# Kernel optimization log

Hardware: AMD Instinct MI355X
Metric: run time of the kernel (lower is better)

## Reference

```python
import jax, jax.numpy as jnp
import numpy as np
import math

B, CH, BINS, W = 2, 8, 1024, 1024
FF = 2048
BANDS = 4
HD = BINS // BANDS
EPS = 1e-5


def _ln(x, g, b):
    m = jnp.mean(x, -1, keepdims=True)
    v = jnp.mean(jnp.square(x - m), -1, keepdims=True)
    return (x - m) * jax.lax.rsqrt(v + EPS) * g + b


def _conv1d(x, w, pad, groups=1):
    # x: [B, C, W], w: [O, I/groups, k]
    return jax.lax.conv_general_dilated(x, w, (1,), [(pad, pad)],
                                        dimension_numbers=('NCH', 'OIH', 'NCH'),
                                        feature_group_count=groups)


def _attn(h, mem, qw, qb, qcw, qcb, kw, kb, kcw, kcb, vw, vb, vcw, vcb, ow, ob, er):
    b, w, c = h.shape

    def proj(src, lw, lb, cw, cb):
        y = src @ lw.T + lb                                   # [b, w, c]
        y = _conv1d(y.transpose(0, 2, 1), cw, 1, groups=c) + cb[None, :, None]
        return y.transpose(0, 2, 1)                           # [b, w, c]

    q = proj(h, qw, qb, qcw, qcb).reshape(b, w, BANDS, HD).transpose(0, 2, 1, 3)   # [b, n, w, hd]
    k = proj(mem, kw, kb, kcw, kcb).reshape(b, w, BANDS, HD).transpose(0, 2, 1, 3)
    v = proj(mem, vw, vb, vcw, vcb).reshape(b, w, BANDS, HD).transpose(0, 2, 1, 3)
    # relative position bias via Music-Transformer pad/skew trick
    p = jnp.einsum('bnwh,hc->bnwc', q, er)                    # [b, n, w, W]
    p = jnp.pad(p, ((0, 0), (0, 0), (0, 0), (1, 0))).transpose(0, 1, 3, 2)[:, :, 1:, :]
    qk = (jnp.einsum('bnqh,bnkh->bnqk', q, k) + p) / math.sqrt(c)
    a = jax.nn.softmax(qk, axis=-1)
    o = jnp.einsum('bnqk,bnkh->bnqh', a, v).transpose(0, 2, 1, 3).reshape(b, w, c)
    return o @ ow.T + ob


def _forward(x, w_in, ln1_g, ln1_b, glu_w, ln2_g, ln2_b, c1L_w, c1R_w, ln3_g, ln3_b,
             c1M_dw, c1M_pw, ln4_g, ln4_b, qw, qb, qcw, qcb, kw, kb, kcw, kcb,
             vw, vb, vcw, vcb, ow, ob, er, ln5_g, ln5_b, c2_w, c3_w):
    # in_project: Linear(channels, 1, bias=False) on x.transpose(1,3), squeeze
    xf = jnp.einsum('bcfw,c->bwf', x, w_in)                   # [B, W, BINS]
    # GLU block
    h = _ln(xf, ln1_g, ln1_b)
    g = h @ glu_w.T
    ga, gb = jnp.split(g, 2, axis=-1)
    xf = xf + ga * jax.nn.sigmoid(gb)
    # conv feedforward block
    h = _ln(xf, ln2_g, ln2_b)
    hL = jax.nn.relu(h @ c1L_w.T)                             # [B, W, FF]
    hR = jax.nn.relu(_conv1d(h.transpose(0, 2, 1), c1R_w, 1)).transpose(0, 2, 1)  # [B, W, FF//4]
    hR = jnp.pad(hR, ((0, 0), (0, 0), (0, FF - FF // 4)))
    h = _ln(hL + hR, ln3_g, ln3_b)
    h = _conv1d(_conv1d(h.transpose(0, 2, 1), c1M_dw, 4, groups=FF), c1M_pw, 0).transpose(0, 2, 1)
    xf = xf + h
    # multiband attention
    h = _ln(xf, ln4_g, ln4_b)
    h = _attn(h, h, qw, qb, qcw, qcb, kw, kb, kcw, kcb, vw, vb, vcw, vcb, ow, ob, er)
    xf = xf + h
    # squared-relu FFN
    h = _ln(xf, ln5_g, ln5_b)
    h = jnp.square(jax.nn.relu(h @ c2_w.T)) @ c3_w.T
    xf = xf + h
    return xf.transpose(0, 2, 1)[:, None, :, :]               # [B, 1, BINS, W]


def setup_inputs() -> dict:
    key = jax.random.key(0)
    keys = iter(jax.random.split(key, 48))

    def n(shape, s=0.02):
        return jax.random.normal(next(keys), shape, dtype=jnp.float32) * s

    ones = lambda d: jnp.ones((d,), jnp.float32)
    zeros = lambda d: jnp.zeros((d,), jnp.float32)
    return {
        'x': jax.random.normal(next(keys), (B, CH, BINS, W), dtype=jnp.float32),
        'w_in': n((CH,)),
        'ln1_g': ones(BINS), 'ln1_b': zeros(BINS),
        'glu_w': n((2 * BINS, BINS)),
        'ln2_g': ones(BINS), 'ln2_b': zeros(BINS),
        'c1L_w': n((FF, BINS)),
        'c1R_w': n((FF // 4, BINS, 3)),
        'ln3_g': ones(FF), 'ln3_b': zeros(FF),
        'c1M_dw': n((FF, 1, 9)),
        'c1M_pw': n((BINS, FF, 1)),
        'ln4_g': ones(BINS), 'ln4_b': zeros(BINS),
        'qw': n((BINS, BINS)), 'qb': zeros(BINS), 'qcw': n((BINS, 1, 3)), 'qcb': zeros(BINS),
        'kw': n((BINS, BINS)), 'kb': zeros(BINS), 'kcw': n((BINS, 1, 3)), 'kcb': zeros(BINS),
        'vw': n((BINS, BINS)), 'vb': zeros(BINS), 'vcw': n((BINS, 1, 3)), 'vcb': zeros(BINS),
        'ow': n((BINS, BINS)), 'ob': zeros(BINS),
        'er': n((HD, W), s=1.0),
        'ln5_g': ones(BINS), 'ln5_b': zeros(BINS),
        'c2_w': n((FF, BINS)), 'c3_w': n((BINS, FF)),
    }


def reference(x, w_in, ln1_g, ln1_b, glu_w, ln2_g, ln2_b, c1L_w, c1R_w, ln3_g, ln3_b,
              c1M_dw, c1M_pw, ln4_g, ln4_b, qw, qb, qcw, qcb, kw, kb, kcw, kcb,
              vw, vb, vcw, vcb, ow, ob, er, ln5_g, ln5_b, c2_w, c3_w):
    return _forward(x, w_in, ln1_g, ln1_b, glu_w, ln2_g, ln2_b, c1L_w, c1R_w, ln3_g, ln3_b,
                    c1M_dw, c1M_pw, ln4_g, ln4_b, qw, qb, qcw, qcb, kw, kb, kcw, kcb,
                    vw, vb, vcw, vcb, ow, ob, er, ln5_g, ln5_b, c2_w, c3_w)
```

## Files before the change

### kernel.cpp

```cpp
#include <hip/hip_runtime.h>


typedef float f32x4 __attribute__((ext_vector_type(4)));
typedef short short8 __attribute__((ext_vector_type(8)));
typedef unsigned short u16;
typedef unsigned int u32;

__device__ __forceinline__ float bf2f(u16 u){
  u32 v = ((u32)u) << 16;
  return __builtin_bit_cast(float, v);
}
__device__ __forceinline__ u16 f2bf(float f){
  u32 u = __builtin_bit_cast(u32, f);
  u32 r = (u + 0x7fffu + ((u >> 16) & 1u)) >> 16;
  return (u16)r;
}
__device__ __forceinline__ u32 pack2(float a, float b){
  return (u32)f2bf(a) | ((u32)f2bf(b) << 16);
}
__device__ __forceinline__ void unpack8(uint4 u, float* f){
  f[0]=bf2f(u.x & 0xffffu); f[1]=bf2f(u.x >> 16);
  f[2]=bf2f(u.y & 0xffffu); f[3]=bf2f(u.y >> 16);
  f[4]=bf2f(u.z & 0xffffu); f[5]=bf2f(u.z >> 16);
  f[6]=bf2f(u.w & 0xffffu); f[7]=bf2f(u.w >> 16);
}

__device__ __forceinline__ void gload16(const u16* g, u16* l){
  __builtin_amdgcn_global_load_lds(
      (const __attribute__((address_space(1))) unsigned int*)g,
      (__attribute__((address_space(3))) unsigned int*)l, 16, 0, 0);
}
template<int N> __device__ __forceinline__ void waitvm(){
  asm volatile("s_waitcnt vmcnt(%0)" :: "n"(N) : "memory");
}
__device__ __forceinline__ void barrier(){ __builtin_amdgcn_s_barrier(); }

template<int ACT, int OB, int MR, int NR, int DUAL, int NBUF>
__global__ __launch_bounds__(256)
void gemm_bt(const u16* __restrict__ A, const u16* __restrict__ Bw,
             const u16* __restrict__ A2, const u16* __restrict__ B2,
             float* __restrict__ Cf, u16* __restrict__ Cb,
             const float* __restrict__ bias, const float* __restrict__ resid,
             int M, int N, int K, int K2,
             int lda, int ldb, int lda2, int ldb2, int ldc,
             int apad, int aoff,
             long aZHi, long aZLo, long bZHi, long bZLo,
             long b2ZHi, long b2ZLo, long cZHi, long cZLo)
{
  constexpr int BM = 32 * MR, BN = 32 * NR;
  constexpr int LPT = MR + NR;
  constexpr int PRE = NBUF - 1;
  __shared__ __align__(16) u16 As[NBUF][BM * 64];
  __shared__ __align__(16) u16 Bs[NBUF][BN * 64];
  const int z = blockIdx.z, zh = z >> 2, zl = z & 3;
  const u16* Az = A + zh * aZHi + zl * aZLo;
  const u16* Bz = Bw + zh * bZHi + zl * bZLo;
  const u16* B2z = DUAL ? (B2 + zh * b2ZHi + zl * b2ZLo) : nullptr;
  const long coff = (long)zh * cZHi + (long)zl * cZLo;
  const int tid = threadIdx.x;
  const int m0 = blockIdx.y * BM, n0 = blockIdx.x * BN;
  const int lane = tid & 63, wid = tid >> 6;
  const int wm = wid >> 1, wn = wid & 1;
  const int lr = lane & 15, lk = lane >> 4;
  const int kA = K >> 6;
  const int NT = kA + (DUAL ? (K2 >> 6) : 0);

  auto stage = [&](int buf, int s){
    #pragma unroll
    for (int i = 0; i < MR; i++){
      int ch = tid + i * 256;
      int r = ch >> 3, c = ch & 7;
      int csw = (c ^ (r & 7)) * 8;
      const u16* src;
      bool d2 = DUAL && (s >= kA);
      if (d2){
        src = A2 + (long)(m0 + r) * lda2 + (s - kA) * 64 + csw;
      } else {
        int gm = m0 + r;
        long ar = (long)gm + (long)(gm >> 10) * apad + aoff;
        src = Az + ar * lda + s * 64 + csw;
      }
      gload16(src, &As[buf][ch * 8]);
    }
    #pragma unroll
    for (int i = 0; i < NR; i++){
      int ch = tid + i * 256;
      int r = ch >> 3, c = ch & 7;
      int csw = (c ^ (r & 7)) * 8;
      const u16* src;
      bool d2 = DUAL && (s >= kA);
      if (d2) src = B2z + (long)(n0 + r) * ldb2 + (s - kA) * 64 + csw;
      else    src = Bz  + (long)(n0 + r) * ldb  + s * 64 + csw;
      gload16(src, &Bs[buf][ch * 8]);
    }
  };

  f32x4 acc[MR][NR];
  #pragma unroll
  for (int i = 0; i < MR; i++)
    #pragma unroll
    for (int j = 0; j < NR; j++) acc[i][j] = f32x4{0.f, 0.f, 0.f, 0.f};

  auto compute = [&](int cur){
    const u16* Ab = &As[cur][0];
    const u16* Bb = &Bs[cur][0];
    short8 av[2][MR], bv[2][NR];
    #pragma unroll
    for (int h = 0; h < 2; h++){
      int g = h * 4 + lk;
      #pragma unroll
      for (int i = 0; i < MR; i++){
        int row = wm * 16 * MR + i * 16 + lr;
        av[h][i] = *(const short8*)(Ab + row * 64 + ((g ^ (row & 7)) * 8));
      }
      #pragma unroll
      for (int j = 0; j < NR; j++){
        int row = wn * 16 * NR + j * 16 + lr;
        bv[h][j] = *(const short8*)(Bb + row * 64 + ((g ^ (row & 7)) * 8));
      }
    }
    #pragma unroll
    for (int h = 0; h < 2; h++)
      #pragma unroll
      for (int i = 0; i < MR; i++)
        #pragma unroll
        for (int j = 0; j < NR; j++)
          acc[i][j] = __builtin_amdgcn_mfma_f32_16x16x32_bf16(av[h][i], bv[h][j], acc[i][j], 0, 0, 0);
  };

  const int npre = NT < PRE ? NT : PRE;
  for (int p = 0; p < npre; p++) stage(p, p);
  int s = 0;
  for (; s < NT - PRE; s++){
    waitvm<(NBUF - 2) * LPT>();
    barrier();
    stage((s + PRE) % NBUF, s + PRE);
    compute(s % NBUF);
    barrier();
  }
  for (; s < NT; s++){
    waitvm<0>();
    barrier();
    compute(s % NBUF);
    barrier();
  }

  float* CfZ = Cf ? Cf + coff : nullptr;
  u16*  CbZ = Cb ? Cb + coff : nullptr;
  const float* rz = resid ? resid + coff : nullptr;
  #pragma unroll
  for (int i = 0; i < MR; i++){
    int rowb = m0 + wm * 16 * MR + i * 16 + lk * 4;
    #pragma unroll
    for (int j = 0; j < NR; j++){
      int colg = n0 + wn * 16 * NR + j * 16 + lr;
      f32x4 v = acc[i][j];
      float bvl = bias ? bias[colg] : 0.f;
      #pragma unroll
      for (int r = 0; r < 4; r++){
        long idx = (long)(rowb + r) * ldc + colg;
        float xv = v[r] + bvl;
        if constexpr (ACT == 1){ xv = fmaxf(xv, 0.f); }
        if constexpr (ACT == 2){ xv = fmaxf(xv, 0.f); xv = xv * xv; }
        if (rz) xv += rz[idx];
        if constexpr (OB) CbZ[idx] = f2bf(xv); else CfZ[idx] = xv;
      }
    }
  }
}

template<int NC>
__global__ __launch_bounds__(256)
void ln_kernel(const float* __restrict__ in, u16* __restrict__ out,
               const float* __restrict__ gg, const float* __restrict__ bb,
               int rowpad, int rowadd)
{
  constexpr int PER = NC / 256;
  const int row = blockIdx.x;
  const float* x = in + (long)row * NC;
  const int tid = threadIdx.x;
  float v[PER];
  #pragma unroll
  for (int i = 0; i < PER; i += 4){
    f32x4 t = *(const f32x4*)(x + tid * PER + i);
    v[i] = t.x; v[i+1] = t.y; v[i+2] = t.z; v[i+3] = t.w;
  }
  float s = 0.f, sq = 0.f;
  #pragma unroll
  for (int i = 0; i < PER; i++){ s += v[i]; sq += v[i] * v[i]; }
  #pragma unroll
  for (int o = 32; o; o >>= 1){ s += __shfl_xor(s, o); sq += __shfl_xor(sq, o); }
  __shared__ float as_[4], aq_[4];
  const int wv = tid >> 6;
  if ((tid & 63) == 0){ as_[wv] = s; aq_[wv] = sq; }
  __syncthreads();
  s  = as_[0] + as_[1] + as_[2] + as_[3];
  sq = aq_[0] + aq_[1] + aq_[2] + aq_[3];
  const float mean = s * (1.f / NC);
  const float var  = sq * (1.f / NC) - mean * mean;
  const float rs = rsqrtf(var + 1e-5f);
  const long orow = (long)row + (long)(row >> 10) * rowpad + rowadd;
  u16* op = out + orow * NC + tid * PER;
  u32 word[PER / 2];
  #pragma unroll
  for (int i = 0; i < PER; i += 2){
    int c = tid * PER + i;
    float y0 = (v[i]   - mean) * rs * gg[c]   + bb[c];
    float y1 = (v[i+1] - mean) * rs * gg[c+1] + bb[c+1];
    word[i / 2] = pack2(y0, y1);
  }
  if constexpr (PER == 4) *(uint2*)op = *(uint2*)word;
  else                    *(uint4*)op = *(uint4*)word;
}

__global__ __launch_bounds__(256)
void inproj_kernel(const float* __restrict__ x, const float* __restrict__ w_in,
                   float* __restrict__ xf)
{
  __shared__ float tile[32][33];
  const int b = blockIdx.z, f0 = blockIdx.x * 32, w0 = blockIdx.y * 32;
  const int tx = threadIdx.x, ty = threadIdx.y;
  float wr[8];
  #pragma unroll
  for (int c = 0; c < 8; c++) wr[c] = w_in[c];
  #pragma unroll
  for (int i = 0; i < 4; i++){
    int f = f0 + ty + i * 8;
    float s = 0.f;
    #pragma unroll
    for (int c = 0; c < 8; c++)
      s += x[(((long)(b * 8 + c)) * 1024 + f) * 1024 + w0 + tx] * wr[c];
    tile[ty + i * 8][tx] = s;
  }
  __syncthreads();
  #pragma unroll
  for (int i = 0; i < 4; i++){
    int wl = ty + i * 8;
    xf[((long)(b * 1024 + w0 + wl)) * 1024 + f0 + tx] = tile[tx][wl];
  }
}

__global__ __launch_bounds__(256)
void tr_out_kernel(const float* __restrict__ xf, float* __restrict__ out)
{
  __shared__ float tile[32][33];
  const int b = blockIdx.z, f0 = blockIdx.x * 32, w0 = blockIdx.y * 32;
  const int tx = threadIdx.x, ty = threadIdx.y;
  #pragma unroll
  for (int i = 0; i < 4; i++)
    tile[ty + i * 8][tx] = xf[((long)(b * 1024 + w0 + ty + i * 8)) * 1024 + f0 + tx];
  __syncthreads();
  #pragma unroll
  for (int i = 0; i < 4; i++)
    out[((long)(b * 1024 + f0 + ty + i * 8)) * 1024 + w0 + tx] = tile[tx][ty + i * 8];
}

__global__ __launch_bounds__(256)
void glu_kernel(const float* __restrict__ g, float* __restrict__ xf)
{
  const long e = (long)blockIdx.x * 256 + threadIdx.x;
  const long row = e >> 8; const int c4 = ((int)e & 255) * 4;
  f32x4 a  = *(const f32x4*)(g + row * 2048 + c4);
  f32x4 bv = *(const f32x4*)(g + row * 2048 + 1024 + c4);
  f32x4 o  = *(f32x4*)(xf + row * 1024 + c4);
  o.x += a.x / (1.f + __expf(-bv.x));
  o.y += a.y / (1.f + __expf(-bv.y));
  o.z += a.z / (1.f + __expf(-bv.z));
  o.w += a.w / (1.f + __expf(-bv.w));
  *(f32x4*)(xf + row * 1024 + c4) = o;
}

__global__ __launch_bounds__(256)
void dwconv9_kernel(const u16* __restrict__ in, u16* __restrict__ out,
                    const float* __restrict__ dwT)
{
  const int id = blockIdx.x * 256 + threadIdx.x;
  const int cg = id & 255;
  const int tg = id >> 8;
  const int c0 = cg * 8;
  const int t0 = tg * 4;
  const int b = t0 >> 10;
  const int w0 = t0 & 1023;
  const u16* bin = in + ((long)b << 10) * 2048 + c0;
  float wt[9][8];
  #pragma unroll
  for (int j = 0; j < 9; j++){
    f32x4 lo = *(const f32x4*)(dwT + j * 2048 + c0);
    f32x4 hi = *(const f32x4*)(dwT + j * 2048 + c0 + 4);
    wt[j][0]=lo.x; wt[j][1]=lo.y; wt[j][2]=lo.z; wt[j][3]=lo.w;
    wt[j][4]=hi.x; wt[j][5]=hi.y; wt[j][6]=hi.z; wt[j][7]=hi.w;
  }
  float win[9][8];
  #pragma unroll
  for (int r = 0; r < 9; r++){
    int wr = w0 - 4 + r;
    if (wr >= 0 && wr < 1024){
      uint4 u = *(const uint4*)(bin + (long)wr * 2048);
      unpack8(u, win[r]);
    } else {
      #pragma unroll
      for (int i = 0; i < 8; i++) win[r][i] = 0.f;
    }
  }
  #pragma unroll
  for (int s = 0; s < 4; s++){
    float acc[8] = {0,0,0,0,0,0,0,0};
    #pragma unroll
    for (int j = 0; j < 9; j++)
      #pragma unroll
      for (int i = 0; i < 8; i++)
        acc[i] += win[(s + j) % 9][i] * wt[j][i];
    uint4 o;
    o.x = pack2(acc[0], acc[1]); o.y = pack2(acc[2], acc[3]);
    o.z = pack2(acc[4], acc[5]); o.w = pack2(acc[6], acc[7]);
    *(uint4*)(out + (long)(t0 + s) * 2048 + c0) = o;
    if (s < 3){
      int wr = w0 + s + 5;
      if (wr < 1024){
        uint4 u = *(const uint4*)(bin + (long)wr * 2048);
        unpack8(u, win[s % 9]);
      } else {
        #pragma unroll
        for (int i = 0; i < 8; i++) win[s % 9][i] = 0.f;
      }
    }
  }
}

__global__ __launch_bounds__(256)
void conv3_kernel(const u16* __restrict__ qin, u16* __restrict__ qout,
                  const float* __restrict__ qwT, const float* __restrict__ qbb,
                  const u16* __restrict__ kin, u16* __restrict__ kout,
                  const float* __restrict__ kwT, const float* __restrict__ kbb,
                  int ld)
{
  const int sel = blockIdx.y;
  const u16* in  = sel ? kin : qin;
  u16* out       = sel ? kout : qout;
  const float* wT = sel ? kwT : qwT;
  const float* bp = sel ? kbb : qbb;
  const int id = blockIdx.x * 256 + threadIdx.x;
  const int cg = id & 127;
  const int tg = id >> 7;
  const int c0 = cg * 8;
  const int t0 = tg * 4;
  const int b = t0 >> 10;
  const int w0 = t0 & 1023;
  const u16* bin = in + ((long)b << 10) * ld + c0;
  float wt[3][8], bias[8];
  #pragma unroll
  for (int j = 0; j < 3; j++){
    f32x4 lo = *(const f32x4*)(wT + j * 1024 + c0);
    f32x4 hi = *(const f32x4*)(wT + j * 1024 + c0 + 4);
    wt[j][0]=lo.x; wt[j][1]=lo.y; wt[j][2]=lo.z; wt[j][3]=lo.w;
    wt[j][4]=hi.x; wt[j][5]=hi.y; wt[j][6]=hi.z; wt[j][7]=hi.w;
  }
  {
    f32x4 lo = *(const f32x4*)(bp + c0);
    f32x4 hi = *(const f32x4*)(bp + c0 + 4);
    bias[0]=lo.x; bias[1]=lo.y; bias[2]=lo.z; bias[3]=lo.w;
    bias[4]=hi.x; bias[5]=hi.y; bias[6]=hi.z; bias[7]=hi.w;
  }
  float win[3][8];
  #pragma unroll
  for (int r = 0; r < 3; r++){
    int wr = w0 - 1 + r;
    if (wr >= 0 && wr < 1024){
      uint4 u = *(const uint4*)(bin + (long)wr * ld);
      unpack8(u, win[r]);
    } else {
      #pragma unroll
      for (int i = 0; i < 8; i++) win[r][i] = 0.f;
    }
  }
  #pragma unroll
  for (int s = 0; s < 4; s++){
    float acc[8];
    #pragma unroll
    for (int i = 0; i < 8; i++) acc[i] = bias[i];
    #pragma unroll
    for (int j = 0; j < 3; j++)
      #pragma unroll
      for (int i = 0; i < 8; i++)
        acc[i] += win[(s + j) % 3][i] * wt[j][i];
    uint4 o;
    o.x = pack2(acc[0], acc[1]); o.y = pack2(acc[2], acc[3]);
    o.z = pack2(acc[4], acc[5]); o.w = pack2(acc[6], acc[7]);
    *(uint4*)(out + (long)(t0 + s) * 1024 + c0) = o;
    if (s < 3){
      int wr = w0 + s + 2;
      if (wr < 1024){
        uint4 u = *(const uint4*)(bin + (long)wr * ld);
        unpack8(u, win[s % 3]);
      } else {
        #pragma unroll
        for (int i = 0; i < 8; i++) win[s % 3][i] = 0.f;
      }
    }
  }
}

__global__ __launch_bounds__(256)
void vconv3t_kernel(const u16* __restrict__ in, u16* __restrict__ out,
                    const float* __restrict__ cw, const float* __restrict__ cb,
                    int ld)
{
  __shared__ float ins[34][33];
  __shared__ float outs[32][33];
  const int b = blockIdx.z, w0 = blockIdx.x * 32, c0 = blockIdx.y * 32;
  const int tx = threadIdx.x, ty = threadIdx.y;
  for (int r = ty; r < 34; r += 8){
    int w = w0 - 1 + r;
    ins[r][tx] = (w >= 0 && w < 1024) ? bf2f(in[((long)(b * 1024 + w)) * ld + c0 + tx]) : 0.f;
  }
  __syncthreads();
  const float wt0 = cw[(c0 + tx) * 3 + 0], wt1 = cw[(c0 + tx) * 3 + 1], wt2 = cw[(c0 + tx) * 3 + 2];
  const float bb = cb[c0 + tx];
  #pragma unroll
  for (int i = 0; i < 4; i++){
    int wl = ty + i * 8;
    outs[wl][tx] = ins[wl][tx] * wt0 + ins[wl + 1][tx] * wt1 + ins[wl + 2][tx] * wt2 + bb;
  }
  __syncthreads();
  #pragma unroll
  for (int i = 0; i < 4; i++){
    int cl = ty + i * 8;
    int c = c0 + cl; int n = c >> 8; int h = c & 255;
    out[((long)((b * 4 + n) * 256 + h)) * 1024 + w0 + tx] = f2bf(outs[tx][cl]);
  }
}

__global__ __launch_bounds__(256)
void softmax_kernel(const float* __restrict__ S, u16* __restrict__ out)
{
  const long row = blockIdx.x;
  const float* x = S + row * 1024;
  const int tid = threadIdx.x;
  f32x4 v = *(const f32x4*)(x + tid * 4);
  v *= 0.03125f;
  float m = fmaxf(fmaxf(v.x, v.y), fmaxf(v.z, v.w));
  #pragma unroll
  for (int o = 32; o; o >>= 1) m = fmaxf(m, __shfl_xor(m, o));
  __shared__ float sm[4], ssum[4];
  const int wv = tid >> 6;
  if ((tid & 63) == 0) sm[wv] = m;
  __syncthreads();
  m = fmaxf(fmaxf(sm[0], sm[1]), fmaxf(sm[2], sm[3]));
  f32x4 e;
  e.x = __expf(v.x - m); e.y = __expf(v.y - m);
  e.z = __expf(v.z - m); e.w = __expf(v.w - m);
  float s = e.x + e.y + e.z + e.w;
  #pragma unroll
  for (int o = 32; o; o >>= 1) s += __shfl_xor(s, o);
  if ((tid & 63) == 0) ssum[wv] = s;
  __syncthreads();
  s = ssum[0] + ssum[1] + ssum[2] + ssum[3];
  const float inv = 1.f / s;
  uint2 o2;
  o2.x = pack2(e.x * inv, e.y * inv);
  o2.y = pack2(e.z * inv, e.w * inv);
  *(uint2*)(out + row * 1024 + tid * 4) = o2;
}

struct Ptrs9 { const float* s[9]; u16* d[9]; };

__global__ __launch_bounds__(256)
void prep_cvt_kernel(Ptrs9 p)
{
  constexpr int n4s[9] = {524288,524288,524288,262144,262144,262144,262144,524288,524288};
  const int job = blockIdx.y;
  const int id = blockIdx.x * 256 + threadIdx.x;
  if (id >= n4s[job]) return;
  f32x4 v = *(const f32x4*)(p.s[job] + (long)id * 4);
  uint2 o; o.x = pack2(v.x, v.y); o.y = pack2(v.z, v.w);
  *(uint2*)(p.d[job] + (long)id * 4) = o;
}

__global__ __launch_bounds__(256)
void prep_misc_kernel(const float* __restrict__ c1R_w, u16* __restrict__ wb_c1R,
                      const float* __restrict__ er, u16* __restrict__ wb_erT,
                      const float* __restrict__ c1M_dw, float* __restrict__ dwT,
                      const float* __restrict__ qcw, float* __restrict__ qcwT,
                      const float* __restrict__ kcw, float* __restrict__ kcwT,
                      const float* __restrict__ qb, const float* __restrict__ kb,
                      const float* __restrict__ vb, float* __restrict__ bqkv,
                      u16* __restrict__ hpad)
{
  const int bid = blockIdx.x;
  const int tid = threadIdx.x;
  if (bid < 6144){
    int id = bid * 256 + tid;
    int oc = id / 3072; int rem = id - oc * 3072;
    int tau = rem >> 10; int ic = rem & 1023;
    wb_c1R[id] = f2bf(c1R_w[(long)oc * 3072 + ic * 3 + tau]);
  } else if (bid < 7168){
    int id = (bid - 6144) * 256 + tid;
    int qi = id >> 8; int h = id & 255;
    wb_erT[id] = f2bf(er[(long)h * 1024 + qi]);
  } else if (bid < 7240){
    int id = (bid - 7168) * 256 + tid;
    int jj = id >> 11; int c = id & 2047;
    dwT[id] = c1M_dw[c * 9 + jj];
  } else if (bid < 7252){
    int id = (bid - 7240) * 256 + tid;
    int jj = id >> 10; int c = id & 1023;
    qcwT[id] = qcw[c * 3 + jj];
  } else if (bid < 7264){
    int id = (bid - 7252) * 256 + tid;
    int jj = id >> 10; int c = id & 1023;
    kcwT[id] = kcw[c * 3 + jj];
  } else if (bid < 7276){
    int id = (bid - 7264) * 256 + tid;
    bqkv[id] = (id < 1024) ? qb[id] : (id < 2048) ? kb[id - 1024] : vb[id - 2048];
  } else {
    int id = (bid - 7276) * 256 + tid;
    int r = id >> 10; int c = id & 1023;
    int b = r >> 1; int edge = r & 1;
    long row = (long)b * 1026 + (edge ? 1025 : 0);
    hpad[row * 1024 + c] = 0;
  }
}

extern "C" void kernel_launch(void* const* d_in, const int* in_sizes, int n_in,
                              void* d_out, int out_size, void* d_ws, size_t ws_size,
                              hipStream_t stream)
{
  (void)in_sizes; (void)n_in; (void)out_size; (void)ws_size;
  const float* x     = (const float*)d_in[0];
  const float* w_in  = (const float*)d_in[1];
  const float* ln1_g = (const float*)d_in[2];
  const float* ln1_b = (const float*)d_in[3];
  const float* glu_w = (const float*)d_in[4];
  const float* ln2_g = (const float*)d_in[5];
  const float* ln2_b = (const float*)d_in[6];
  const float* c1L_w = (const float*)d_in[7];
  const float* c1R_w = (const float*)d_in[8];
  const float* ln3_g = (const float*)d_in[9];
  const float* ln3_b = (const float*)d_in[10];
  const float* c1M_dw= (const float*)d_in[11];
  const float* c1M_pw= (const float*)d_in[12];
  const float* ln4_g = (const float*)d_in[13];
  const float* ln4_b = (const float*)d_in[14];
  const float* qw  = (const float*)d_in[15];
  const float* qb  = (const float*)d_in[16];
  const float* qcw = (const float*)d_in[17];
  const float* qcb = (const float*)d_in[18];
  const float* kw  = (const float*)d_in[19];
  const float* kb  = (const float*)d_in[20];
  const float* kcw = (const float*)d_in[21];
  const float* kcb = (const float*)d_in[22];
  const float* vw  = (const float*)d_in[23];
  const float* vb  = (const float*)d_in[24];
  const float* vcw = (const float*)d_in[25];
  const float* vcb = (const float*)d_in[26];
  const float* ow  = (const float*)d_in[27];
  const float* ob  = (const float*)d_in[28];
  const float* er  = (const float*)d_in[29];
  const float* ln5_g = (const float*)d_in[30];
  const float* ln5_b = (const float*)d_in[31];
  const float* c2_w  = (const float*)d_in[32];
  const float* c3_w  = (const float*)d_in[33];
  float* out = (float*)d_out;

  const long TT = 2048;
  char* wsb = (char*)d_ws;
  size_t off = 0;
  auto alloc = [&](size_t bytes) -> char* {
    char* p = wsb + off;
    off = (off + bytes + 255) & ~(size_t)255;
    return p;
  };
  float* XF     = (float*)alloc(TT * 1024 * 4);
  u16* wb_glu = (u16*)alloc(2048L * 1024 * 2);
  u16* wb_c1L = (u16*)alloc(2048L * 1024 * 2);
  u16* wb_c1R = (u16*)alloc(512L * 3072 * 2);
  u16* wb_pw  = (u16*)alloc(1024L * 2048 * 2);
  u16* wb_q   = (u16*)alloc(1024L * 1024 * 2);
  u16* wb_k   = (u16*)alloc(1024L * 1024 * 2);
  u16* wb_v   = (u16*)alloc(1024L * 1024 * 2);
  u16* wb_ow  = (u16*)alloc(1024L * 1024 * 2);
  u16* wb_c2  = (u16*)alloc(2048L * 1024 * 2);
  u16* wb_c3  = (u16*)alloc(1024L * 2048 * 2);
  u16* wb_erT = (u16*)alloc(1024L * 256 * 2);
  float* dwT  = (float*)alloc(9L * 2048 * 4);
  float* qcwT = (float*)alloc(3L * 1024 * 4);
  float* kcwT = (float*)alloc(3L * 1024 * 4);
  float* bqkv = (float*)alloc(3072L * 4);
  u16* HPAD   = (u16*)alloc(2L * 1026 * 1024 * 2);
  u16* LNA    = (u16*)alloc(TT * 1024 * 2);
  float* R16f = (float*)alloc(8L * 1024 * 1024 * 4);
  u16* R8     = (u16*)alloc(8L * 1024 * 1024 * 2);
  u16* LN3O = R8;
  u16* DW9O = R8 + TT * 2048;
  u16* SBF  = R8;
  u16* C2O  = R8;
  u16* qkvbuf = (u16*)alloc(TT * 3072 * 2);
  u16* q2b  = (u16*)alloc(TT * 1024 * 2);
  u16* k2b  = (u16*)alloc(TT * 1024 * 2);
  u16* v2T  = (u16*)alloc(8L * 256 * 1024 * 2);
  u16* obuf = qkvbuf;

  Ptrs9 pj;
  pj.s[0]=glu_w; pj.d[0]=wb_glu;
  pj.s[1]=c1L_w; pj.d[1]=wb_c1L;
  pj.s[2]=c1M_pw; pj.d[2]=wb_pw;
  pj.s[3]=qw; pj.d[3]=wb_q;
  pj.s[4]=kw; pj.d[4]=wb_k;
  pj.s[5]=vw; pj.d[5]=wb_v;
  pj.s[6]=ow; pj.d[6]=wb_ow;
  pj.s[7]=c2_w; pj.d[7]=wb_c2;
  pj.s[8]=c3_w; pj.d[8]=wb_c3;
  prep_cvt_kernel<<<dim3(2048, 9), 256, 0, stream>>>(pj);
  prep_misc_kernel<<<7292, 256, 0, stream>>>(c1R_w, wb_c1R, er, wb_erT, c1M_dw, dwT,
                                             qcw, qcwT, kcw, kcwT, qb, kb, vb, bqkv, HPAD);

  inproj_kernel<<<dim3(32, 32, 2), dim3(32, 8), 0, stream>>>(x, w_in, XF);

  ln_kernel<1024><<<2048, 256, 0, stream>>>(XF, LNA, ln1_g, ln1_b, 0, 0);
  gemm_bt<0,0,4,2,0,2><<<dim3(32,16,1), 256, 0, stream>>>(LNA, wb_glu, nullptr, nullptr,
      R16f, nullptr, nullptr, nullptr,
      2048, 2048, 1024, 0, 1024, 1024, 0, 0, 2048, 0, 0, 0,0,0,0,0,0,0,0);
  glu_kernel<<<2048, 256, 0, stream>>>(R16f, XF);

  ln_kernel<1024><<<2048, 256, 0, stream>>>(XF, HPAD, ln2_g, ln2_b, 2, 1);
  gemm_bt<1,0,4,2,0,2><<<dim3(32,16,1), 256, 0, stream>>>(HPAD, wb_c1L, nullptr, nullptr,
      R16f, nullptr, nullptr, nullptr,
      2048, 2048, 1024, 0, 1024, 1024, 0, 0, 2048, 2, 1, 0,0,0,0,0,0,0,0);
  gemm_bt<1,0,2,2,0,4><<<dim3(8,32,1), 256, 0, stream>>>(HPAD, wb_c1R, nullptr, nullptr,
      R16f, nullptr, nullptr, R16f,
      2048, 512, 3072, 0, 1024, 3072, 0, 0, 2048, 2, 0, 0,0,0,0,0,0,0,0);
  ln_kernel<2048><<<2048, 256, 0, stream>>>(R16f, LN3O, ln3_g, ln3_b, 0, 0);
  dwconv9_kernel<<<512, 256, 0, stream>>>(LN3O, DW9O, dwT);
  gemm_bt<0,0,2,2,0,3><<<dim3(16,32,1), 256, 0, stream>>>(DW9O, wb_pw, nullptr, nullptr,
      XF, nullptr, nullptr, XF,
      2048, 1024, 2048, 0, 2048, 2048, 0, 0, 1024, 0, 0, 0,0,0,0,0,0,0,0);

  ln_kernel<1024><<<2048, 256, 0, stream>>>(XF, LNA, ln4_g, ln4_b, 0, 0);
  gemm_bt<0,1,4,2,0,2><<<dim3(48,16,1), 256, 0, stream>>>(LNA, wb_q, nullptr, nullptr,
      nullptr, qkvbuf, bqkv, nullptr,
      2048, 3072, 1024, 0, 1024, 1024, 0, 0, 3072, 0, 0, 0,0,0,0,0,0,0,0);
  conv3_kernel<<<dim3(256,2), 256, 0, stream>>>(qkvbuf, q2b, qcwT, qcb,
                                                qkvbuf + 1024, k2b, kcwT, kcb, 3072);
  vconv3t_kernel<<<dim3(32, 32, 2), dim3(32, 8), 0, stream>>>(qkvbuf + 2048, v2T, vcw, vcb, 3072);
  gemm_bt<0,0,4,2,1,2><<<dim3(16,8,8), 256, 0, stream>>>(q2b, k2b, wb_erT, q2b,
      R16f, nullptr, nullptr, nullptr,
      1024, 1024, 256, 256, 1024, 1024, 256, 1024, 1024, 0, 0,
      1048576, 256, 1048576, 256, 1048576, 256, 4194304, 1048576);
  softmax_kernel<<<8192, 256, 0, stream>>>(R16f, SBF);
  gemm_bt<0,1,2,2,0,3><<<dim3(4,16,8), 256, 0, stream>>>(SBF, v2T, nullptr, nullptr,
      nullptr, obuf, nullptr, nullptr,
      1024, 256, 1024, 0, 1024, 1024, 0, 0, 1024, 0, 0,
      4194304, 1048576, 1048576, 262144, 0, 0, 1048576, 256);
  gemm_bt<0,0,2,2,0,3><<<dim3(16,32,1), 256, 0, stream>>>(obuf, wb_ow, nullptr, nullptr,
      XF, nullptr, ob, XF,
      2048, 1024, 1024, 0, 1024, 1024, 0, 0, 1024, 0, 0, 0,0,0,0,0,0,0,0);

  ln_kernel<1024><<<2048, 256, 0, stream>>>(XF, LNA, ln5_g, ln5_b, 0, 0);
  gemm_bt<2,1,4,2,0,2><<<dim3(32,16,1), 256, 0, stream>>>(LNA, wb_c2, nullptr, nullptr,
      nullptr, C2O, nullptr, nullptr,
      2048, 2048, 1024, 0, 1024, 1024, 0, 0, 2048, 0, 0, 0,0,0,0,0,0,0,0);
  gemm_bt<0,0,2,2,0,3><<<dim3(16,32,1), 256, 0, stream>>>(C2O, wb_c3, nullptr, nullptr,
      XF, nullptr, nullptr, XF,
      2048, 1024, 2048, 0, 2048, 2048, 0, 0, 1024, 0, 0, 0,0,0,0,0,0,0,0);

  tr_out_kernel<<<dim3(32, 32, 2), dim3(32, 8), 0, stream>>>(XF, out);
}
```

Baseline: 315.1 us.

## Fuse GLU into its GEMM and store intermediates in bf16

Adds a dedicated GLU GEMM that computes the value and gate halves together and applies the sigmoid gating plus residual directly into XF, which removes the fp32 GLU scratch buffer and the separate glu kernel. The conv-feedforward hidden activations and the attention score matrix are now stored as bf16 instead of fp32. The score scaling moves into the GEMM epilogue, and softmax runs in place on the bf16 buffer. This cuts global memory traffic and one launch, at the cost of bf16 rounding before the softmax and the LayerNorm. A few pipeline depths also change from 2 to 3 buffers.

```diff
diff --git a/kernel.cpp b/kernel.cpp
--- a/kernel.cpp
+++ b/kernel.cpp
@@ -35,12 +35,12 @@
 }
 __device__ __forceinline__ void barrier(){ __builtin_amdgcn_s_barrier(); }
 
-template<int ACT, int OB, int MR, int NR, int DUAL, int NBUF>
+template<int ACT, int OB, int MR, int NR, int DUAL, int NBUF, int RB, int SC>
 __global__ __launch_bounds__(256)
 void gemm_bt(const u16* __restrict__ A, const u16* __restrict__ Bw,
              const u16* __restrict__ A2, const u16* __restrict__ B2,
              float* __restrict__ Cf, u16* __restrict__ Cb,
-             const float* __restrict__ bias, const float* __restrict__ resid,
+             const float* __restrict__ bias, const void* __restrict__ resid,
              int M, int N, int K, int K2,
              int lda, int ldb, int lda2, int ldb2, int ldc,
              int apad, int aoff,
@@ -147,7 +147,8 @@
 
   float* CfZ = Cf ? Cf + coff : nullptr;
   u16*  CbZ = Cb ? Cb + coff : nullptr;
-  const float* rz = resid ? resid + coff : nullptr;
+  const float* rzf = (!RB && resid) ? ((const float*)resid) + coff : nullptr;
+  const u16*  rzb = (RB && resid) ? ((const u16*)resid) + coff : nullptr;
   #pragma unroll
   for (int i = 0; i < MR; i++){
     int rowb = m0 + wm * 16 * MR + i * 16 + lk * 4;
@@ -162,28 +163,146 @@
         float xv = v[r] + bvl;
         if constexpr (ACT == 1){ xv = fmaxf(xv, 0.f); }
         if constexpr (ACT == 2){ xv = fmaxf(xv, 0.f); xv = xv * xv; }
-        if (rz) xv += rz[idx];
+        if constexpr (SC){ xv *= 0.03125f; }
+        if constexpr (RB){ if (rzb) xv += bf2f(rzb[idx]); }
+        else             { if (rzf) xv += rzf[idx]; }
         if constexpr (OB) CbZ[idx] = f2bf(xv); else CfZ[idx] = xv;
       }
     }
   }
 }
 
-template<int NC>
-__global__ __launch_bounds__(256)
-void ln_kernel(const float* __restrict__ in, u16* __restrict__ out,
+template<int NBUF>
+__global__ __launch_bounds__(256)
+void gemm_glu(const u16* __restrict__ A, const u16* __restrict__ Bw,
+              float* __restrict__ XF)
+{
+  constexpr int LPT = 6;
+  constexpr int PRE = NBUF - 1;
+  constexpr int NT = 16;
+  __shared__ __align__(16) u16 As[NBUF][64 * 64];
+  __shared__ __align__(16) u16 Bs[NBUF][128 * 64];
+  const int tid = threadIdx.x;
+  const int m0 = blockIdx.y * 64, n0 = blockIdx.x * 64;
+  const int lane = tid & 63, wid = tid >> 6;
+  const int wm = wid >> 1, wn = wid & 1;
+  const int lr = lane & 15, lk = lane >> 4;
+
+  auto stage = [&](int buf, int s){
+    #pragma unroll
+    for (int i = 0; i < 2; i++){
+      int ch = tid + i * 256;
+      int r = ch >> 3, c = ch & 7;
+      int csw = (c ^ (r & 7)) * 8;
+      gload16(A + (long)(m0 + r) * 1024 + s * 64 + csw, &As[buf][ch * 8]);
+    }
+    #pragma unroll
+    for (int i = 0; i < 4; i++){
+      int ch = tid + i * 256;
+      int r = ch >> 3, c = ch & 7;
+      int csw = (c ^ (r & 7)) * 8;
+      int grow = (r < 64) ? (n0 + r) : (1024 + n0 + r - 64);
+      gload16(Bw + (long)grow * 1024 + s * 64 + csw, &Bs[buf][ch * 8]);
+    }
+  };
+
+  f32x4 accv[2][2], accg[2][2];
+  #pragma unroll
+  for (int i = 0; i < 2; i++)
+    #pragma unroll
+    for (int j = 0; j < 2; j++){
+      accv[i][j] = f32x4{0.f,0.f,0.f,0.f};
+      accg[i][j] = f32x4{0.f,0.f,0.f,0.f};
+    }
+
+  auto compute = [&](int cur){
+    const u16* Ab = &As[cur][0];
+    const u16* Bb = &Bs[cur][0];
+    short8 av[2][2], bvv[2][2], bvg[2][2];
+    #pragma unroll
+    for (int h = 0; h < 2; h++){
+      int g = h * 4 + lk;
+      #pragma unroll
+      for (int i = 0; i < 2; i++){
+        int row = wm * 32 + i * 16 + lr;
+        av[h][i] = *(const short8*)(Ab + row * 64 + ((g ^ (row & 7)) * 8));
+      }
+      #pragma unroll
+      for (int j = 0; j < 2; j++){
+        int row = wn * 32 + j * 16 + lr;
+        bvv[h][j] = *(const short8*)(Bb + row * 64 + ((g ^ (row & 7)) * 8));
+        int rowg = 64 + row;
+        bvg[h][j] = *(const short8*)(Bb + rowg * 64 + ((g ^ (rowg & 7)) * 8));
+      }
+    }
+    #pragma unroll
+    for (int h = 0; h < 2; h++)
+      #pragma unroll
+      for (int i = 0; i < 2; i++)
+        #pragma unroll
+        for (int j = 0; j < 2; j++){
+          accv[i][j] = __builtin_amdgcn_mfma_f32_16x16x32_bf16(av[h][i], bvv[h][j], accv[i][j], 0, 0, 0);
+          accg[i][j] = __builtin_amdgcn_mfma_f32_16x16x32_bf16(av[h][i], bvg[h][j], accg[i][j], 0, 0, 0);
+        }
+  };
+
+  const int npre = NT < PRE ? NT : PRE;
+  for (int p = 0; p < npre; p++) stage(p, p);
+  int s = 0;
+  for (; s < NT - PRE; s++){
+    waitvm<(NBUF - 2) * LPT>();
+    barrier();
+    stage((s + PRE) % NBUF, s + PRE);
+    compute(s % NBUF);
+    barrier();
+  }
+  for (; s < NT; s++){
+    waitvm<0>();
+    barrier();
+    compute(s % NBUF);
+    barrier();
+  }
+
+  #pragma unroll
+  for (int i = 0; i < 2; i++){
+    int rowb = m0 + wm * 32 + i * 16 + lk * 4;
+    #pragma unroll
+    for (int j = 0; j < 2; j++){
+      int colg = n0 + wn * 32 + j * 16 + lr;
+      #pragma unroll
+      for (int r = 0; r < 4; r++){
+        long idx = (long)(rowb + r) * 1024 + colg;
+        float g = accg[i][j][r];
+        XF[idx] += accv[i][j][r] / (1.f + __expf(-g));
+      }
+    }
+  }
+}
+
+template<int NC, int INBF>
+__global__ __launch_bounds__(256)
+void ln_kernel(const void* __restrict__ in, u16* __restrict__ out,
                const float* __restrict__ gg, const float* __restrict__ bb,
                int rowpad, int rowadd)
 {
   constexpr int PER = NC / 256;
   const int row = blockIdx.x;
-  const float* x = in + (long)row * NC;
   const int tid = threadIdx.x;
   float v[PER];
-  #pragma unroll
-  for (int i = 0; i < PER; i += 4){
-    f32x4 t = *(const f32x4*)(x + tid * PER + i);
-    v[i] = t.x; v[i+1] = t.y; v[i+2] = t.z; v[i+3] = t.w;
+  if constexpr (INBF){
+    const u16* x = ((const u16*)in) + (long)row * NC + tid * PER;
+    #pragma unroll
+    for (int i = 0; i < PER; i += 8){
+      uint4 u = *(const uint4*)(x + i);
+      unpack8(u, &v[i]);
+    }
+  } else {
+    const float* x = ((const float*)in) + (long)row * NC + tid * PER;
+    #pragma unroll
+    for (int i = 0; i < PER; i += 4){
+      f32x4 t = *(const f32x4*)(x + i);
+      v[i] = t.x; v[i+1] = t.y; v[i+2] = t.z; v[i+3] = t.w;
+    }
   }
   float s = 0.f, sq = 0.f;
   #pragma unroll
@@ -253,21 +372,6 @@
   #pragma unroll
   for (int i = 0; i < 4; i++)
     out[((long)(b * 1024 + f0 + ty + i * 8)) * 1024 + w0 + tx] = tile[tx][ty + i * 8];
-}
-
-__global__ __launch_bounds__(256)
-void glu_kernel(const float* __restrict__ g, float* __restrict__ xf)
-{
-  const long e = (long)blockIdx.x * 256 + threadIdx.x;
-  const long row = e >> 8; const int c4 = ((int)e & 255) * 4;
-  f32x4 a  = *(const f32x4*)(g + row * 2048 + c4);
-  f32x4 bv = *(const f32x4*)(g + row * 2048 + 1024 + c4);
-  f32x4 o  = *(f32x4*)(xf + row * 1024 + c4);
-  o.x += a.x / (1.f + __expf(-bv.x));
-  o.y += a.y / (1.f + __expf(-bv.y));
-  o.z += a.z / (1.f + __expf(-bv.z));
-  o.w += a.w / (1.f + __expf(-bv.w));
-  *(f32x4*)(xf + row * 1024 + c4) = o;
 }
 
 __global__ __launch_bounds__(256)
@@ -431,14 +535,15 @@
 }
 
 __global__ __launch_bounds__(256)
-void softmax_kernel(const float* __restrict__ S, u16* __restrict__ out)
+void softmax_kernel(u16* __restrict__ buf)
 {
   const long row = blockIdx.x;
-  const float* x = S + row * 1024;
   const int tid = threadIdx.x;
-  f32x4 v = *(const f32x4*)(x + tid * 4);
-  v *= 0.03125f;
-  float m = fmaxf(fmaxf(v.x, v.y), fmaxf(v.z, v.w));
+  u16* p = buf + row * 1024 + tid * 4;
+  uint2 u = *(const uint2*)p;
+  float v0 = bf2f(u.x & 0xffffu), v1 = bf2f(u.x >> 16);
+  float v2 = bf2f(u.y & 0xffffu), v3 = bf2f(u.y >> 16);
+  float m = fmaxf(fmaxf(v0, v1), fmaxf(v2, v3));
   #pragma unroll
   for (int o = 32; o; o >>= 1) m = fmaxf(m, __shfl_xor(m, o));
   __shared__ float sm[4], ssum[4];
@@ -446,10 +551,9 @@
   if ((tid & 63) == 0) sm[wv] = m;
   __syncthreads();
   m = fmaxf(fmaxf(sm[0], sm[1]), fmaxf(sm[2], sm[3]));
-  f32x4 e;
-  e.x = __expf(v.x - m); e.y = __expf(v.y - m);
-  e.z = __expf(v.z - m); e.w = __expf(v.w - m);
-  float s = e.x + e.y + e.z + e.w;
+  float e0 = __expf(v0 - m), e1 = __expf(v1 - m);
+  float e2 = __expf(v2 - m), e3 = __expf(v3 - m);
+  float s = e0 + e1 + e2 + e3;
   #pragma unroll
   for (int o = 32; o; o >>= 1) s += __shfl_xor(s, o);
   if ((tid & 63) == 0) ssum[wv] = s;
@@ -457,9 +561,9 @@
   s = ssum[0] + ssum[1] + ssum[2] + ssum[3];
   const float inv = 1.f / s;
   uint2 o2;
-  o2.x = pack2(e.x * inv, e.y * inv);
-  o2.y = pack2(e.z * inv, e.w * inv);
-  *(uint2*)(out + row * 1024 + tid * 4) = o2;
+  o2.x = pack2(e0 * inv, e1 * inv);
+  o2.y = pack2(e2 * inv, e3 * inv);
+  *(uint2*)p = o2;
 }
 
 struct Ptrs9 { const float* s[9]; u16* d[9]; };
@@ -570,7 +674,7 @@
     off = (off + bytes + 255) & ~(size_t)255;
     return p;
   };
-  float* XF     = (float*)alloc(TT * 1024 * 4);
+  float* XF   = (float*)alloc(TT * 1024 * 4);
   u16* wb_glu = (u16*)alloc(2048L * 1024 * 2);
   u16* wb_c1L = (u16*)alloc(2048L * 1024 * 2);
   u16* wb_c1R = (u16*)alloc(512L * 3072 * 2);
@@ -588,17 +692,16 @@
   float* bqkv = (float*)alloc(3072L * 4);
   u16* HPAD   = (u16*)alloc(2L * 1026 * 1024 * 2);
   u16* LNA    = (u16*)alloc(TT * 1024 * 2);
-  float* R16f = (float*)alloc(8L * 1024 * 1024 * 4);
-  u16* R8     = (u16*)alloc(8L * 1024 * 1024 * 2);
-  u16* LN3O = R8;
-  u16* DW9O = R8 + TT * 2048;
-  u16* SBF  = R8;
-  u16* C2O  = R8;
+  u16* HS     = (u16*)alloc(TT * 2048 * 2);
+  u16* LN3O   = (u16*)alloc(TT * 2048 * 2);
+  u16* DW9O   = (u16*)alloc(TT * 2048 * 2);
+  u16* SBF    = (u16*)alloc(8L * 1024 * 1024 * 2);
   u16* qkvbuf = (u16*)alloc(TT * 3072 * 2);
   u16* q2b  = (u16*)alloc(TT * 1024 * 2);
   u16* k2b  = (u16*)alloc(TT * 1024 * 2);
   u16* v2T  = (u16*)alloc(8L * 256 * 1024 * 2);
   u16* obuf = qkvbuf;
+  u16* C2O  = LN3O;
 
   Ptrs9 pj;
   pj.s[0]=glu_w; pj.d[0]=wb_glu;
@@ -616,50 +719,47 @@
 
   inproj_kernel<<<dim3(32, 32, 2), dim3(32, 8), 0, stream>>>(x, w_in, XF);
 
-  ln_kernel<1024><<<2048, 256, 0, stream>>>(XF, LNA, ln1_g, ln1_b, 0, 0);
-  gemm_bt<0,0,4,2,0,2><<<dim3(32,16,1), 256, 0, stream>>>(LNA, wb_glu, nullptr, nullptr,
-      R16f, nullptr, nullptr, nullptr,
-      2048, 2048, 1024, 0, 1024, 1024, 0, 0, 2048, 0, 0, 0,0,0,0,0,0,0,0);
-  glu_kernel<<<2048, 256, 0, stream>>>(R16f, XF);
-
-  ln_kernel<1024><<<2048, 256, 0, stream>>>(XF, HPAD, ln2_g, ln2_b, 2, 1);
-  gemm_bt<1,0,4,2,0,2><<<dim3(32,16,1), 256, 0, stream>>>(HPAD, wb_c1L, nullptr, nullptr,
-      R16f, nullptr, nullptr, nullptr,
+  ln_kernel<1024,0><<<2048, 256, 0, stream>>>(XF, LNA, ln1_g, ln1_b, 0, 0);
+  gemm_glu<3><<<dim3(16,32,1), 256, 0, stream>>>(LNA, wb_glu, XF);
+
+  ln_kernel<1024,0><<<2048, 256, 0, stream>>>(XF, HPAD, ln2_g, ln2_b, 2, 1);
+  gemm_bt<1,1,4,2,0,3,0,0><<<dim3(32,16,1), 256, 0, stream>>>(HPAD, wb_c1L, nullptr, nullptr,
+      nullptr, HS, nullptr, nullptr,
       2048, 2048, 1024, 0, 1024, 1024, 0, 0, 2048, 2, 1, 0,0,0,0,0,0,0,0);
-  gemm_bt<1,0,2,2,0,4><<<dim3(8,32,1), 256, 0, stream>>>(HPAD, wb_c1R, nullptr, nullptr,
-      R16f, nullptr, nullptr, R16f,
+  gemm_bt<1,1,2,2,0,4,1,0><<<dim3(8,32,1), 256, 0, stream>>>(HPAD, wb_c1R, nullptr, nullptr,
+      nullptr, HS, nullptr, HS,
       2048, 512, 3072, 0, 1024, 3072, 0, 0, 2048, 2, 0, 0,0,0,0,0,0,0,0);
-  ln_kernel<2048><<<2048, 256, 0, stream>>>(R16f, LN3O, ln3_g, ln3_b, 0, 0);
+  ln_kernel<2048,1><<<2048, 256, 0, stream>>>(HS, LN3O, ln3_g, ln3_b, 0, 0);
   dwconv9_kernel<<<512, 256, 0, stream>>>(LN3O, DW9O, dwT);
-  gemm_bt<0,0,2,2,0,3><<<dim3(16,32,1), 256, 0, stream>>>(DW9O, wb_pw, nullptr, nullptr,
+  gemm_bt<0,0,2,2,0,3,0,0><<<dim3(16,32,1), 256, 0, stream>>>(DW9O, wb_pw, nullptr, nullptr,
       XF, nullptr, nullptr, XF,
       2048, 1024, 2048, 0, 2048, 2048, 0, 0, 1024, 0, 0, 0,0,0,0,0,0,0,0);
 
-  ln_kernel<1024><<<2048, 256, 0, stream>>>(XF, LNA, ln4_g, ln4_b, 0, 0);
-  gemm_bt<0,1,4,2,0,2><<<dim3(48,16,1), 256, 0, stream>>>(LNA, wb_q, nullptr, nullptr,
+  ln_kernel<1024,0><<<2048, 256, 0, stream>>>(XF, LNA, ln4_g, ln4_b, 0, 0);
+  gemm_bt<0,1,4,2,0,2,0,0><<<dim3(48,16,1), 256, 0, stream>>>(LNA, wb_q, nullptr, nullptr,
       nullptr, qkvbuf, bqkv, nullptr,
       2048, 3072, 1024, 0, 1024, 1024, 0, 0, 3072, 0, 0, 0,0,0,0,0,0,0,0);
   conv3_kernel<<<dim3(256,2), 256, 0, stream>>>(qkvbuf, q2b, qcwT, qcb,
                                                 qkvbuf + 1024, k2b, kcwT, kcb, 3072);
   vconv3t_kernel<<<dim3(32, 32, 2), dim3(32, 8), 0, stream>>>(qkvbuf + 2048, v2T, vcw, vcb, 3072);
-  gemm_bt<0,0,4,2,1,2><<<dim3(16,8,8), 256, 0, stream>>>(q2b, k2b, wb_erT, q2b,
-      R16f, nullptr, nullptr, nullptr,
+  gemm_bt<0,1,4,2,1,2,0,1><<<dim3(16,8,8), 256, 0, stream>>>(q2b, k2b, wb_erT, q2b,
+      nullptr, SBF, nullptr, nullptr,
       1024, 1024, 256, 256, 1024, 1024, 256, 1024, 1024, 0, 0,
       1048576, 256, 1048576, 256, 1048576, 256, 4194304, 1048576);
-  softmax_kernel<<<8192, 256, 0, stream>>>(R16f, SBF);
-  gemm_bt<0,1,2,2,0,3><<<dim3(4,16,8), 256, 0, stream>>>(SBF, v2T, nullptr, nullptr,
+  softmax_kernel<<<8192, 256, 0, stream>>>(SBF);
+  gemm_bt<0,1,2,2,0,3,0,0><<<dim3(4,16,8), 256, 0, stream>>>(SBF, v2T, nullptr, nullptr,
       nullptr, obuf, nullptr, nullptr,
       1024, 256, 1024, 0, 1024, 1024, 0, 0, 1024, 0, 0,
       4194304, 1048576, 1048576, 262144, 0, 0, 1048576, 256);
-  gemm_bt<0,0,2,2,0,3><<<dim3(16,32,1), 256, 0, stream>>>(obuf, wb_ow, nullptr, nullptr,
+  gemm_bt<0,0,2,2,0,3,0,0><<<dim3(16,32,1), 256, 0, stream>>>(obuf, wb_ow, nullptr, nullptr,
       XF, nullptr, ob, XF,
       2048, 1024, 1024, 0, 1024, 1024, 0, 0, 1024, 0, 0, 0,0,0,0,0,0,0,0);
 
-  ln_kernel<1024><<<2048, 256, 0, stream>>>(XF, LNA, ln5_g, ln5_b, 0, 0);
-  gemm_bt<2,1,4,2,0,2><<<dim3(32,16,1), 256, 0, stream>>>(LNA, wb_c2, nullptr, nullptr,
+  ln_kernel<1024,0><<<2048, 256, 0, stream>>>(XF, LNA, ln5_g, ln5_b, 0, 0);
+  gemm_bt<2,1,4,2,0,3,0,0><<<dim3(32,16,1), 256, 0, stream>>>(LNA, wb_c2, nullptr, nullptr,
       nullptr, C2O, nullptr, nullptr,
       2048, 2048, 1024, 0, 1024, 1024, 0, 0, 2048, 0, 0, 0,0,0,0,0,0,0,0);
-  gemm_bt<0,0,2,2,0,3><<<dim3(16,32,1), 256, 0, stream>>>(C2O, wb_c3, nullptr, nullptr,
+  gemm_bt<0,0,2,2,0,3,0,0><<<dim3(16,32,1), 256, 0, stream>>>(C2O, wb_c3, nullptr, nullptr,
       XF, nullptr, nullptr, XF,
       2048, 1024, 2048, 0, 2048, 2048, 0, 0, 1024, 0, 0, 0,0,0,0,0,0,0,0);
 
```

Result: no change. 310.3 us (-1.5%).
